# Performance work log

Hardware: AMD Instinct MI355X
Metric: run time of the kernel (lower is better)

The kernel has to match this reference:

```python
import jax, jax.numpy as jnp
import numpy as np

N_FREQ = 50  # n_frequencies in Model.__init__


def _sine_tables(n_freq):
    i = np.arange(1, n_freq + 1, dtype=np.float32)
    base = 1.0 / (1000.0 ** (2.0 * i / n_freq))           # [n_freq]
    freqs = np.repeat(base, 2)                             # [2*n_freq]
    shifts = np.tile(np.array([0.0, np.pi / 2], dtype=np.float32), n_freq)  # [2*n_freq]
    return jnp.asarray(freqs), jnp.asarray(shifts)


def setup_inputs() -> dict:
    key = jax.random.key(0)
    ks = jax.random.split(key, 8)
    n_frag, n_genes, d_sine, d_emb = 200000, 500, 4 * N_FREQ, 10
    cell_n, gene_n = 200, 500
    coordinates = jax.random.normal(ks[0], (n_frag, 2), dtype=jnp.float32) * 1000.0
    stdv = 1.0 / np.sqrt(d_emb)
    w1 = jax.random.uniform(ks[1], (n_genes, d_sine, d_emb), jnp.float32, -stdv, stdv)
    b1 = jnp.zeros((n_genes, d_emb), jnp.float32)
    w2 = jnp.ones((n_genes, d_emb), jnp.float32)
    b2 = jnp.zeros((n_genes,), jnp.float32)
    genemapping = jax.random.randint(ks[2], (n_frag,), 0, n_genes, dtype=jnp.int64 if jax.config.jax_enable_x64 else jnp.int32)
    local_cellxgene_ix = jax.random.randint(ks[3], (n_frag,), 0, cell_n * gene_n, dtype=genemapping.dtype)
    genes_oi = jnp.arange(gene_n, dtype=genemapping.dtype)
    return {
        "coordinates": coordinates, "w1": w1, "b1": b1, "w2": w2, "b2": b2,
        "genemapping": genemapping, "local_cellxgene_ix": local_cellxgene_ix,
        "genes_oi": genes_oi, "cell_n": cell_n, "gene_n": gene_n,
    }


def reference(coordinates, w1, b1, w2, b2, genemapping, local_cellxgene_ix, genes_oi, cell_n, gene_n):
    freqs, shifts = _sine_tables(N_FREQ)
    n_frag = coordinates.shape[0]
    # SineEncoding: [n_frag, 2, 2*n_freq] -> [n_frag, 4*n_freq]
    emb = jnp.sin(coordinates[..., None] * freqs + shifts).reshape(n_frag, -1)
    # FragmentEmbedder: per-fragment gene-specific linear + sigmoid
    h = jnp.einsum('fs,fsd->fd', emb, w1[genemapping]) + b1[genemapping]
    h = jax.nn.sigmoid(h)
    # EmbeddingGenePooler: scatter-sum into cell x gene bins
    pooled = jax.ops.segment_sum(h, local_cellxgene_ix, num_segments=cell_n * gene_n)
    cge = pooled.reshape(cell_n, gene_n, -1)
    # EmbeddingToExpression: gene-specific dot + bias
    out = (cge * w2[genes_oi]).sum(-1) + b2[genes_oi]
    return out
```

## Files before the change

### kernel.cpp

```cpp
#include <hip/hip_runtime.h>
#include <hip/hip_bf16.h>
#include <math.h>

#define NF    50
#define DEMB  10
#define W1G   (4 * NF * DEMB)
#define MAXG  512

#define HTPB   256
#define HCHUNK 4096
#define HFPT   (HCHUNK / HTPB)

#define KPAD  232
#define HPAD  19
#define W2PAD 11
#define ARENA 7680

typedef __attribute__((ext_vector_type(8))) short short8v;
typedef __attribute__((ext_vector_type(4))) float f32x4v;

__device__ __forceinline__ short f2bf(float f) {
    unsigned u = __float_as_uint(f);
    u += 0x7fffu + ((u >> 16) & 1u);
    return (short)(u >> 16);
}

__global__ __launch_bounds__(HTPB) void hist_init_k(
    const int* __restrict__ gm, int n_frag, int n_genes,
    int* __restrict__ counts_mat,
    float* __restrict__ out, const float* __restrict__ b2,
    const int* __restrict__ genes_oi, int gene_n, int total)
{
    __shared__ int lcnt[MAXG];
    for (int t = threadIdx.x; t < MAXG; t += HTPB) lcnt[t] = 0;
    __syncthreads();

    int base = blockIdx.x * HCHUNK;
#pragma unroll
    for (int j = 0; j < HFPT; ++j) {
        int f = base + j * HTPB + (int)threadIdx.x;
        if (f < n_frag) atomicAdd(&lcnt[gm[f]], 1);
    }

    int nthreads = gridDim.x * HTPB;
    for (int i = blockIdx.x * HTPB + (int)threadIdx.x; i < total; i += nthreads) {
        int col = (int)((unsigned)i % (unsigned)gene_n);
        out[i] = b2[genes_oi[col]];
    }

    __syncthreads();
    int* row = counts_mat + (size_t)blockIdx.x * MAXG;
    for (int t = threadIdx.x; t < MAXG; t += HTPB) row[t] = lcnt[t];
}

__global__ void scan_k(const int* __restrict__ counts_mat, int nblk,
                       int* __restrict__ po, int* __restrict__ cursor,
                       int* __restrict__ cnt, int* __restrict__ w2g,
                       int n_genes, int wmax)
{
    __shared__ int buf[MAXG];
    int tid = threadIdx.x;
    int s = 0;
#pragma unroll 8
    for (int b = 0; b < nblk; ++b) s += counts_mat[(size_t)b * MAXG + tid];
    int pc = ((s + 63) >> 6) << 6;
    buf[tid] = pc;
    __syncthreads();
    for (int d = 1; d < MAXG; d <<= 1) {
        int t = (tid >= d) ? buf[tid - d] : 0;
        __syncthreads();
        buf[tid] += t;
        __syncthreads();
    }
    int incl = buf[tid];
    if (tid < n_genes) {
        po[tid + 1] = incl;
        cursor[tid] = incl - pc;
        cnt[tid]    = s;
        int wbeg = (incl - pc) >> 6;
        int wend = incl >> 6;
        for (int w = wbeg; w < wend; ++w) w2g[w] = tid;
    }
    if (tid == 0) po[0] = 0;
    __syncthreads();
    int W = buf[n_genes - 1] >> 6;
    for (int w = W + tid; w < wmax; w += MAXG) w2g[w] = -1;
}

__global__ __launch_bounds__(HTPB) void scatter_k(
    const int* __restrict__ gm, const float* __restrict__ coords,
    const int* __restrict__ lcg, int* __restrict__ cursor,
    float* __restrict__ xs, int* __restrict__ bins,
    int n_frag, int n_genes)
{
    __shared__ int lcnt[MAXG];
    __shared__ int lbase[MAXG];
    for (int t = threadIdx.x; t < MAXG; t += HTPB) lcnt[t] = 0;
    __syncthreads();

    int base = blockIdx.x * HCHUNK;
    int g[HFPT], lr[HFPT];
#pragma unroll
    for (int j = 0; j < HFPT; ++j) {
        int f = base + j * HTPB + (int)threadIdx.x;
        if (f < n_frag) {
            g[j]  = gm[f];
            lr[j] = atomicAdd(&lcnt[g[j]], 1);
        } else {
            g[j] = -1;
        }
    }
    __syncthreads();
    for (int t = threadIdx.x; t < MAXG; t += HTPB) {
        int c = lcnt[t];
        lbase[t] = c ? atomicAdd(&cursor[t], c) : 0;
    }
    __syncthreads();
#pragma unroll
    for (int j = 0; j < HFPT; ++j) {
        if (g[j] >= 0) {
            int f = base + j * HTPB + (int)threadIdx.x;
            int pos = lbase[g[j]] + lr[j];
            float2 xy = ((const float2*)coords)[f];
            xs[2 * pos + 0] = xy.x;
            xs[2 * pos + 1] = xy.y;
            bins[pos] = lcg[f];
        }
    }
}

__global__ __launch_bounds__(256) void main_mfma_k(
    const float* __restrict__ w1, const float* __restrict__ b1,
    const float* __restrict__ w2, const int* __restrict__ genes_oi,
    const float* __restrict__ xs, const int* __restrict__ bins,
    const int* __restrict__ po, const int* __restrict__ cnt,
    const int* __restrict__ w2g, float* __restrict__ out,
    int gene_n, int wmax)
{
    __shared__ float fr[NF];
    __shared__ float w2l[MAXG * W2PAD];
    __shared__ __align__(16) char arena[4][ARENA];

    if (threadIdx.x < NF) {
        float ex = (-2.0f * (float)(threadIdx.x + 1) / (float)NF) * 9.965784284662087f;
        fr[threadIdx.x] = exp2f(ex) * 0.15915494309189535f;
    }
    for (int c = threadIdx.x; c < gene_n; c += 256) {
        int gi = genes_oi[c];
#pragma unroll
        for (int dd = 0; dd < DEMB; ++dd)
            w2l[c * W2PAD + dd] = w2[(size_t)gi * DEMB + dd];
    }
    __syncthreads();

    int wid  = threadIdx.x >> 6;
    int lane = threadIdx.x & 63;
    int fw   = blockIdx.x * 4 + wid;

    int g = (fw < wmax) ? w2g[fw] : -1;
    g = __builtin_amdgcn_readfirstlane(g);
    if (g < 0) return;

    int d  = lane & 15;
    int q  = lane >> 4;
    int dc = (d < 10) ? d : 9;

    int start = po[g];
    int count = cnt[g];
    int pos   = fw * 64 + lane;
    bool valid = (pos - start) < count;
    float2 xy = valid ? ((const float2*)xs)[pos] : make_float2(0.0f, 0.0f);
    int bin_own = valid ? bins[pos] : 0;
    int col_own = (int)((unsigned)bin_own % (unsigned)gene_n);

    short* Bw = (short*)(arena[wid]);
    const float* wg = w1 + (size_t)g * W1G;
#pragma unroll
    for (int r = 0; r < 8; ++r) {
        int e4 = r * 64 + lane;
        if (e4 < W1G / 4) {
            float4 v = ((const float4*)wg)[e4];
            int e = e4 * 4;
            int k0 = e / 10, d0 = e - k0 * 10;
#pragma unroll
            for (int c = 0; c < 4; ++c) {
                Bw[d0 * KPAD + k0] = f2bf((&v.x)[c]);
                d0++; if (d0 == 10) { d0 = 0; k0++; }
            }
        }
    }
    for (int idx = lane; idx < 320; idx += 64) {
        int row = idx >> 5, kz = 200 + (idx & 31);
        Bw[row * KPAD + kz] = 0;
    }

    short8v breg[7];
    {
        const char* bp = arena[wid] + dc * (KPAD * 2) + q * 16;
#pragma unroll
        for (int kk = 0; kk < 7; ++kk)
            breg[kk] = *(const short8v*)(bp + kk * 64);
    }

    float b1v = b1[(size_t)g * DEMB + dc];
    f32x4v acc[4];
#pragma unroll
    for (int m = 0; m < 4; ++m) { acc[m][0] = b1v; acc[m][1] = b1v; acc[m][2] = b1v; acc[m][3] = b1v; }

#pragma unroll
    for (int m = 0; m < 4; ++m) {
        int srcA = m * 16 + d;
        float ax = __shfl(xy.x, srcA);
        float ay = __shfl(xy.y, srcA);
#pragma unroll
        for (int kk = 0; kk < 7; ++kk) {
            short8v afrag;
#pragma unroll
            for (int jj = 0; jj < 4; ++jj) {
                int k0 = kk * 32 + q * 8 + 2 * jj;
                int cc = (k0 >= 100) ? 1 : 0;
                int ii = (k0 - cc * 100) >> 1;
                ii = (k0 < 200) ? ii : 0;
                float fv = fr[ii];
                float xv = cc ? ay : ax;
                float r = xv * fv; r -= rintf(r);
                afrag[2 * jj]     = f2bf(__builtin_amdgcn_sinf(r));
                afrag[2 * jj + 1] = f2bf(__builtin_amdgcn_cosf(r));
            }
            acc[m] = __builtin_amdgcn_mfma_f32_16x16x32_bf16(afrag, breg[kk], acc[m], 0, 0, 0);
        }
    }

    float* hb = (float*)(arena[wid]);
#pragma unroll
    for (int m = 0; m < 4; ++m)
#pragma unroll
        for (int r = 0; r < 4; ++r)
            hb[(m * 16 + q * 4 + r) * HPAD + d] = acc[m][r];

    float sum = 0.0f;
    const float* wrow2 = &w2l[col_own * W2PAD];
#pragma unroll
    for (int dd = 0; dd < DEMB; ++dd) {
        float hv = hb[lane * HPAD + dd];
        float sg = 1.0f / (1.0f + __expf(-hv));
        sum += sg * wrow2[dd];
    }
    if (valid) atomicAdd(&out[bin_own], sum);
}

__global__ __launch_bounds__(256) void frag_naive_k(
    const float* __restrict__ coords, const float* __restrict__ w1,
    const float* __restrict__ b1, const float* __restrict__ w2,
    const int* __restrict__ gm, const int* __restrict__ lcg,
    const int* __restrict__ genes_oi, float* __restrict__ out,
    int gene_n, int n_frag)
{
    __shared__ float fr[NF];
    if (threadIdx.x < NF) {
        float ex = (-2.0f * (float)(threadIdx.x + 1) / (float)NF) * 9.965784284662087f;
        fr[threadIdx.x] = exp2f(ex) * 0.15915494309189535f;
    }
    __syncthreads();

    int f = blockIdx.x * blockDim.x + threadIdx.x;
    if (f >= n_frag) return;
    int g = gm[f];
    const float* wrow  = w1 + (size_t)g * W1G;
    const float* b1row = b1 + (size_t)g * DEMB;
    float x0 = coords[2 * f + 0];
    float x1 = coords[2 * f + 1];

    float h[DEMB];
#pragma unroll
    for (int d = 0; d < DEMB; ++d) h[d] = b1row[d];
#pragma unroll 2
    for (int i = 0; i < NF; ++i) {
        float fv = fr[i];
        float r0 = x0 * fv; r0 -= rintf(r0);
        float r1 = x1 * fv; r1 -= rintf(r1);
        float s0 = __builtin_amdgcn_sinf(r0), c0 = __builtin_amdgcn_cosf(r0);
        float s1 = __builtin_amdgcn_sinf(r1), c1 = __builtin_amdgcn_cosf(r1);
        const float* wa = wrow + (2 * i) * DEMB;
        const float* wb = wrow + (2 * NF + 2 * i) * DEMB;
#pragma unroll
        for (int d = 0; d < DEMB; ++d) {
            h[d] += s0 * wa[d] + c0 * wa[DEMB + d] + s1 * wb[d] + c1 * wb[DEMB + d];
        }
    }
    int bin = lcg[f];
    int col = (int)((unsigned)bin % (unsigned)gene_n);
    const float* w2row = w2 + (size_t)genes_oi[col] * DEMB;
    float sum = 0.0f;
#pragma unroll
    for (int d = 0; d < DEMB; ++d) {
        float sg = 1.0f / (1.0f + __expf(-h[d]));
        sum += sg * w2row[d];
    }
    atomicAdd(&out[bin], sum);
}

__global__ void init_out_k(float* __restrict__ out, const float* __restrict__ b2,
                           const int* __restrict__ genes_oi, int gene_n, int total)
{
    int i = blockIdx.x * blockDim.x + threadIdx.x;
    if (i < total) {
        int col = (int)((unsigned)i % (unsigned)gene_n);
        out[i] = b2[genes_oi[col]];
    }
}

extern "C" void kernel_launch(void* const* d_in, const int* in_sizes, int n_in,
                              void* d_out, int out_size, void* d_ws, size_t ws_size,
                              hipStream_t stream)
{
    const float* coords   = (const float*)d_in[0];
    const float* w1       = (const float*)d_in[1];
    const float* b1       = (const float*)d_in[2];
    const float* w2       = (const float*)d_in[3];
    const float* b2       = (const float*)d_in[4];
    const int*   gm       = (const int*)d_in[5];
    const int*   lcg      = (const int*)d_in[6];
    const int*   genes_oi = (const int*)d_in[7];

    int n_frag  = in_sizes[5];
    int n_genes = in_sizes[4];
    int gene_n  = in_sizes[7];
    int total   = out_size;
    float* out  = (float*)d_out;

    int nblk = (n_frag + HCHUNK - 1) / HCHUNK;
    int wmax = (n_frag >> 6) + n_genes + 1;
    size_t padcap = (size_t)n_frag + 64 * (size_t)n_genes + 64;

    int* counts_mat = (int*)d_ws;
    int* po         = counts_mat + (size_t)nblk * MAXG;
    int* cursor     = po + (MAXG + 1);
    int* cnt        = cursor + MAXG;
    int* w2g        = cnt + MAXG;
    float* xs       = (float*)(w2g + wmax);
    int* bins       = (int*)(xs + 2 * padcap);
    size_t need = ((size_t)nblk * MAXG + (MAXG + 1) + 2 * MAXG + wmax
                   + 3 * padcap) * sizeof(int);

    bool use_sorted = (ws_size >= need) && (n_genes <= MAXG);
    if (use_sorted) {
        hist_init_k<<<nblk, HTPB, 0, stream>>>(gm, n_frag, n_genes, counts_mat,
                                               out, b2, genes_oi, gene_n, total);
        scan_k<<<1, MAXG, 0, stream>>>(counts_mat, nblk, po, cursor, cnt, w2g,
                                       n_genes, wmax);
        scatter_k<<<nblk, HTPB, 0, stream>>>(gm, coords, lcg, cursor,
                                             xs, bins, n_frag, n_genes);
        int mblk = (wmax + 3) / 4;
        main_mfma_k<<<mblk, 256, 0, stream>>>(w1, b1, w2, genes_oi, xs, bins,
                                              po, cnt, w2g, out, gene_n, wmax);
    } else {
        init_out_k<<<(total + 255) / 256, 256, 0, stream>>>(out, b2, genes_oi, gene_n, total);
        frag_naive_k<<<(n_frag + 255) / 256, 256, 0, stream>>>(coords, w1, b1, w2, gm, lcg,
                                                               genes_oi, out, gene_n, n_frag);
    }
}
```

Measured before the change: 49.89 us.

## Pre-transpose w1 to bf16 once per gene and shrink main kernel LDS

Each gene's w1 block is now converted to bf16 and transposed once, inside the histogram kernel, which is launched with enough blocks to cover all genes. Previously every wavefront redid this conversion through shared memory, and there are several wavefronts per gene. The main MFMA kernel now loads B fragments straight from global memory and drops the per-block w2 staging and the large arena. That cuts LDS use so it can declare 4 blocks per CU, and it precomputes a frequency table read as float4. The costs are extra workspace, uncached global reads of w2 per lane, and more work in the first kernel.

```diff
diff --git a/kernel.cpp b/kernel.cpp
--- a/kernel.cpp
+++ b/kernel.cpp
@@ -11,35 +11,61 @@
 #define HCHUNK 4096
 #define HFPT   (HCHUNK / HTPB)
 
-#define KPAD  232
-#define HPAD  19
-#define W2PAD 11
-#define ARENA 7680
+#define HPAD  11
+#define TKP   208
 
 typedef __attribute__((ext_vector_type(8))) short short8v;
+typedef __attribute__((ext_vector_type(4))) unsigned int uint4v;
 typedef __attribute__((ext_vector_type(4))) float f32x4v;
 
 __device__ __forceinline__ short f2bf(float f) {
-    unsigned u = __float_as_uint(f);
-    u += 0x7fffu + ((u >> 16) & 1u);
-    return (short)(u >> 16);
+    union { __hip_bfloat16 b; unsigned short u; } v;
+    v.b = __float2bfloat16(f);
+    return (short)v.u;
+}
+__device__ __forceinline__ unsigned pkbf(float lo, float hi) {
+    union { __hip_bfloat162 b; unsigned u; } v;
+    v.b = __float22bfloat162_rn(make_float2(lo, hi));
+    return v.u;
 }
 
 __global__ __launch_bounds__(HTPB) void hist_init_k(
-    const int* __restrict__ gm, int n_frag, int n_genes,
+    const int* __restrict__ gm, const float* __restrict__ w1,
+    short* __restrict__ w1T, int n_frag, int n_genes, int nblk,
     int* __restrict__ counts_mat,
     float* __restrict__ out, const float* __restrict__ b2,
     const int* __restrict__ genes_oi, int gene_n, int total)
 {
     __shared__ int lcnt[MAXG];
+    __shared__ __align__(16) short tile[DEMB][TKP];
+
+    bool do_hist = (int)blockIdx.x < nblk;
+    bool do_tr   = (int)blockIdx.x < n_genes;
+
     for (int t = threadIdx.x; t < MAXG; t += HTPB) lcnt[t] = 0;
     __syncthreads();
 
-    int base = blockIdx.x * HCHUNK;
-#pragma unroll
-    for (int j = 0; j < HFPT; ++j) {
-        int f = base + j * HTPB + (int)threadIdx.x;
-        if (f < n_frag) atomicAdd(&lcnt[gm[f]], 1);
+    if (do_hist) {
+        int base = blockIdx.x * HCHUNK;
+#pragma unroll
+        for (int j = 0; j < HFPT; ++j) {
+            int f = base + j * HTPB + (int)threadIdx.x;
+            if (f < n_frag) atomicAdd(&lcnt[gm[f]], 1);
+        }
+    }
+
+    if (do_tr) {
+        const float* wg = w1 + (size_t)blockIdx.x * W1G;
+        for (int e4 = threadIdx.x; e4 < W1G / 4; e4 += HTPB) {
+            float4 v = ((const float4*)wg)[e4];
+            int e = e4 * 4;
+            int k0 = e / 10, d0 = e - k0 * 10;
+#pragma unroll
+            for (int c = 0; c < 4; ++c) {
+                tile[d0][k0] = f2bf((&v.x)[c]);
+                d0++; if (d0 == 10) { d0 = 0; k0++; }
+            }
+        }
     }
 
     int nthreads = gridDim.x * HTPB;
@@ -47,10 +73,23 @@
         int col = (int)((unsigned)i % (unsigned)gene_n);
         out[i] = b2[genes_oi[col]];
     }
-
-    __syncthreads();
-    int* row = counts_mat + (size_t)blockIdx.x * MAXG;
-    for (int t = threadIdx.x; t < MAXG; t += HTPB) row[t] = lcnt[t];
+    if (blockIdx.x == 0 && threadIdx.x < 64)
+        w1T[(size_t)n_genes * 2000 + threadIdx.x] = 0;
+
+    __syncthreads();
+
+    if (do_hist) {
+        int* row = counts_mat + (size_t)blockIdx.x * MAXG;
+        for (int t = threadIdx.x; t < MAXG; t += HTPB) row[t] = lcnt[t];
+    }
+    if (do_tr) {
+        short* og = w1T + (size_t)blockIdx.x * 2000;
+        for (int o = threadIdx.x; o < 250; o += HTPB) {
+            int dd = o / 25;
+            int off = (o - dd * 25) * 8;
+            *(short8v*)(og + dd * 200 + off) = *(const short8v*)&tile[dd][off];
+        }
+    }
 }
 
 __global__ void scan_k(const int* __restrict__ counts_mat, int nblk,
@@ -129,27 +168,22 @@
     }
 }
 
-__global__ __launch_bounds__(256) void main_mfma_k(
-    const float* __restrict__ w1, const float* __restrict__ b1,
+__global__ __launch_bounds__(256, 4) void main_mfma_k(
+    const short* __restrict__ w1T, const float* __restrict__ b1,
     const float* __restrict__ w2, const int* __restrict__ genes_oi,
     const float* __restrict__ xs, const int* __restrict__ bins,
     const int* __restrict__ po, const int* __restrict__ cnt,
     const int* __restrict__ w2g, float* __restrict__ out,
     int gene_n, int wmax)
 {
-    __shared__ float fr[NF];
-    __shared__ float w2l[MAXG * W2PAD];
-    __shared__ __align__(16) char arena[4][ARENA];
-
-    if (threadIdx.x < NF) {
-        float ex = (-2.0f * (float)(threadIdx.x + 1) / (float)NF) * 9.965784284662087f;
-        fr[threadIdx.x] = exp2f(ex) * 0.15915494309189535f;
-    }
-    for (int c = threadIdx.x; c < gene_n; c += 256) {
-        int gi = genes_oi[c];
-#pragma unroll
-        for (int dd = 0; dd < DEMB; ++dd)
-            w2l[c * W2PAD + dd] = w2[(size_t)gi * DEMB + dd];
+    __shared__ __align__(16) float fr_ext[116];
+    __shared__ __align__(16) float hb_all[4][64 * HPAD];
+
+    if (threadIdx.x < 116) {
+        int i = threadIdx.x;
+        int im = (i < 50) ? i : ((i < 100) ? i - 50 : i - 100);
+        float ex = (-2.0f * (float)(im + 1) / (float)NF) * 9.965784284662087f;
+        fr_ext[i] = exp2f(ex) * 0.15915494309189535f;
     }
     __syncthreads();
 
@@ -173,34 +207,16 @@
     int bin_own = valid ? bins[pos] : 0;
     int col_own = (int)((unsigned)bin_own % (unsigned)gene_n);
 
-    short* Bw = (short*)(arena[wid]);
-    const float* wg = w1 + (size_t)g * W1G;
-#pragma unroll
-    for (int r = 0; r < 8; ++r) {
-        int e4 = r * 64 + lane;
-        if (e4 < W1G / 4) {
-            float4 v = ((const float4*)wg)[e4];
-            int e = e4 * 4;
-            int k0 = e / 10, d0 = e - k0 * 10;
-#pragma unroll
-            for (int c = 0; c < 4; ++c) {
-                Bw[d0 * KPAD + k0] = f2bf((&v.x)[c]);
-                d0++; if (d0 == 10) { d0 = 0; k0++; }
-            }
-        }
-    }
-    for (int idx = lane; idx < 320; idx += 64) {
-        int row = idx >> 5, kz = 200 + (idx & 31);
-        Bw[row * KPAD + kz] = 0;
-    }
-
+    const short* bp = w1T + (size_t)g * 2000 + dc * 200 + q * 8;
     short8v breg[7];
-    {
-        const char* bp = arena[wid] + dc * (KPAD * 2) + q * 16;
-#pragma unroll
-        for (int kk = 0; kk < 7; ++kk)
-            breg[kk] = *(const short8v*)(bp + kk * 64);
-    }
+#pragma unroll
+    for (int kk = 0; kk < 7; ++kk)
+        breg[kk] = *(const short8v*)(bp + kk * 32);
+
+    float4 frv[7];
+#pragma unroll
+    for (int kk = 0; kk < 7; ++kk)
+        frv[kk] = *(const float4*)&fr_ext[16 * kk + 4 * q];
 
     float b1v = b1[(size_t)g * DEMB + dc];
     f32x4v acc[4];
@@ -214,37 +230,46 @@
         float ay = __shfl(xy.y, srcA);
 #pragma unroll
         for (int kk = 0; kk < 7; ++kk) {
-            short8v afrag;
+            uint4v au;
 #pragma unroll
             for (int jj = 0; jj < 4; ++jj) {
-                int k0 = kk * 32 + q * 8 + 2 * jj;
-                int cc = (k0 >= 100) ? 1 : 0;
-                int ii = (k0 - cc * 100) >> 1;
-                ii = (k0 < 200) ? ii : 0;
-                float fv = fr[ii];
-                float xv = cc ? ay : ax;
+                int idx = 16 * kk + 4 * q + jj;
+                float fv = (&frv[kk].x)[jj];
+                float xv = (idx < 50) ? ax : ay;
                 float r = xv * fv; r -= rintf(r);
-                afrag[2 * jj]     = f2bf(__builtin_amdgcn_sinf(r));
-                afrag[2 * jj + 1] = f2bf(__builtin_amdgcn_cosf(r));
+                float sv = __builtin_amdgcn_sinf(r);
+                float cv = __builtin_amdgcn_cosf(r);
+                if (kk == 6) {
+                    bool pad = (idx >= 100);
+                    sv = pad ? 0.0f : sv;
+                    cv = pad ? 0.0f : cv;
+                }
+                au[jj] = pkbf(sv, cv);
             }
+            short8v afrag = __builtin_bit_cast(short8v, au);
             acc[m] = __builtin_amdgcn_mfma_f32_16x16x32_bf16(afrag, breg[kk], acc[m], 0, 0, 0);
         }
     }
 
-    float* hb = (float*)(arena[wid]);
-#pragma unroll
-    for (int m = 0; m < 4; ++m)
-#pragma unroll
-        for (int r = 0; r < 4; ++r)
-            hb[(m * 16 + q * 4 + r) * HPAD + d] = acc[m][r];
-
+    float* hb = hb_all[wid];
+    if (d < 10) {
+#pragma unroll
+        for (int m = 0; m < 4; ++m)
+#pragma unroll
+            for (int r = 0; r < 4; ++r)
+                hb[(m * 16 + q * 4 + r) * HPAD + d] = acc[m][r];
+    }
+
+    int gi = genes_oi[col_own];
+    const float* w2r = w2 + (size_t)gi * DEMB;
     float sum = 0.0f;
-    const float* wrow2 = &w2l[col_own * W2PAD];
-#pragma unroll
-    for (int dd = 0; dd < DEMB; ++dd) {
-        float hv = hb[lane * HPAD + dd];
-        float sg = 1.0f / (1.0f + __expf(-hv));
-        sum += sg * wrow2[dd];
+#pragma unroll
+    for (int p2 = 0; p2 < 5; ++p2) {
+        float2 wv = *(const float2*)(w2r + 2 * p2);
+        float h0 = hb[lane * HPAD + 2 * p2];
+        float h1 = hb[lane * HPAD + 2 * p2 + 1];
+        sum += wv.x / (1.0f + __expf(-h0));
+        sum += wv.y / (1.0f + __expf(-h1));
     }
     if (valid) atomicAdd(&out[bin_own], sum);
 }
@@ -333,26 +358,30 @@
     int wmax = (n_frag >> 6) + n_genes + 1;
     size_t padcap = (size_t)n_frag + 64 * (size_t)n_genes + 64;
 
-    int* counts_mat = (int*)d_ws;
+    short* w1T      = (short*)d_ws;
+    size_t w1T_sh   = (size_t)n_genes * 2000 + 64;
+    int* counts_mat = (int*)(w1T + w1T_sh);
     int* po         = counts_mat + (size_t)nblk * MAXG;
     int* cursor     = po + (MAXG + 1);
     int* cnt        = cursor + MAXG;
     int* w2g        = cnt + MAXG;
     float* xs       = (float*)(w2g + wmax);
     int* bins       = (int*)(xs + 2 * padcap);
-    size_t need = ((size_t)nblk * MAXG + (MAXG + 1) + 2 * MAXG + wmax
+    size_t need = w1T_sh * sizeof(short)
+                + ((size_t)nblk * MAXG + (MAXG + 1) + 2 * MAXG + wmax
                    + 3 * padcap) * sizeof(int);
 
     bool use_sorted = (ws_size >= need) && (n_genes <= MAXG);
     if (use_sorted) {
-        hist_init_k<<<nblk, HTPB, 0, stream>>>(gm, n_frag, n_genes, counts_mat,
-                                               out, b2, genes_oi, gene_n, total);
+        int g1 = (nblk > n_genes) ? nblk : n_genes;
+        hist_init_k<<<g1, HTPB, 0, stream>>>(gm, w1, w1T, n_frag, n_genes, nblk,
+                                             counts_mat, out, b2, genes_oi, gene_n, total);
         scan_k<<<1, MAXG, 0, stream>>>(counts_mat, nblk, po, cursor, cnt, w2g,
                                        n_genes, wmax);
         scatter_k<<<nblk, HTPB, 0, stream>>>(gm, coords, lcg, cursor,
                                              xs, bins, n_frag, n_genes);
         int mblk = (wmax + 3) / 4;
-        main_mfma_k<<<mblk, 256, 0, stream>>>(w1, b1, w2, genes_oi, xs, bins,
+        main_mfma_k<<<mblk, 256, 0, stream>>>(w1T, b1, w2, genes_oi, xs, bins,
                                               po, cnt, w2g, out, gene_n, wmax);
     } else {
         init_out_k<<<(total + 255) / 256, 256, 0, stream>>>(out, b2, genes_oi, gene_n, total);
```

Result: faster. 46.01 us (-7.8%).
